# Kernel tuning notes

Hardware: AMD Instinct MI355X
Metric: run time of the kernel (lower is better)

The kernel has to match this reference:

```python
import jax, jax.numpy as jnp
import numpy as np

N_NODES = 100000
N_GRAPHS = 64


def gcn_layer(x, src, dst, W, b, n):
    # GCNConv: h = x @ W; out_i = sum_j norm_ij * h_j (+ self loop), + bias
    h = x @ W
    deg = jax.ops.segment_sum(jnp.ones(src.shape[0], x.dtype), dst, num_segments=n)
    dinv = jnp.where(deg > 0, jax.lax.rsqrt(deg), 0.0)
    norm = dinv[src] * dinv[dst]                      # [E+N]
    agg = jax.ops.segment_sum(h[src] * norm[:, None], dst, num_segments=n)
    return agg + b


def setup_inputs() -> dict:
    key = jax.random.key(0)
    ks = jax.random.split(key, 12)
    nfeat, nhid, nclass = 128, 64, 10
    E = 1600000
    x = jax.random.normal(ks[0], (N_NODES, nfeat), dtype=jnp.float32)
    edge_index = jax.random.randint(ks[1], (2, E), 0, N_NODES, dtype=jnp.int64)
    batch = jnp.sort(jax.random.randint(ks[2], (N_NODES,), 0, N_GRAPHS, dtype=jnp.int64))
    def w(k, fi, fo):
        return jax.random.normal(k, (fi, fo), dtype=jnp.float32) / np.sqrt(fi)
    return {
        "x": x, "edge_index": edge_index, "batch": batch,
        "W1": w(ks[3], nfeat, nhid), "b1": jnp.zeros((nhid,), jnp.float32),
        "W2": w(ks[4], nhid, nhid), "b2": jnp.zeros((nhid,), jnp.float32),
        "W3": w(ks[5], nhid, nhid), "b3": jnp.zeros((nhid,), jnp.float32),
        "Wl": w(ks[6], nhid, nclass), "bl": jnp.zeros((nclass,), jnp.float32),
    }


def reference(x, edge_index, batch, W1, b1, W2, b2, W3, b3, Wl, bl):
    n = x.shape[0]
    loop = jnp.arange(n, dtype=edge_index.dtype)
    src = jnp.concatenate([edge_index[0], loop])   # self-loops appended
    dst = jnp.concatenate([edge_index[1], loop])
    h = x  # eval mode: dropout is identity; use_bn=False
    for W, b in ((W1, b1), (W2, b2), (W3, b3)):
        h = jax.nn.relu(gcn_layer(h, src, dst, W, b, n))
    # global mean pool per graph
    sums = jax.ops.segment_sum(h, batch, num_segments=N_GRAPHS)
    cnts = jax.ops.segment_sum(jnp.ones((n,), h.dtype), batch, num_segments=N_GRAPHS)
    pooled = sums / jnp.maximum(cnts, 1.0)[:, None]   # [G, nhid]
    logits = pooled @ Wl + bl
    return jax.nn.softmax(logits, axis=1)
```

## Files before the change

kernel.cpp:

```cpp
#include <hip/hip_runtime.h>
#include <math.h>


typedef __attribute__((ext_vector_type(8))) short bf16x8;
typedef __attribute__((ext_vector_type(4))) float f32x4;
typedef __attribute__((ext_vector_type(2))) float f32x2;

__device__ __forceinline__ unsigned short f2bf(float f) {
    unsigned int u = __float_as_uint(f);
    u += 0x7fffu + ((u >> 16) & 1u);
    return (unsigned short)(u >> 16);
}
__device__ __forceinline__ float bf2f(unsigned short u) {
    return __uint_as_float((unsigned int)u << 16);
}
__device__ __forceinline__ float bflo(unsigned int u) {
    return __uint_as_float(u << 16);
}
__device__ __forceinline__ float bfhi(unsigned int u) {
    return __uint_as_float(u & 0xffff0000u);
}


__global__ __launch_bounds__(256) void hist_kernel(const int* __restrict__ dst,
                                                   int* __restrict__ counts,
                                                   int E, int P, int C,
                                                   const float* __restrict__ W1,
                                                   const float* __restrict__ W2,
                                                   const float* __restrict__ W3,
                                                   unsigned short* __restrict__ Wt1,
                                                   unsigned short* __restrict__ Wt2,
                                                   unsigned short* __restrict__ Wt3,
                                                   float* __restrict__ sums, int G) {
    int t = threadIdx.x, b = blockIdx.x;
    if (b >= 256) {
        int xb = b - 256;
        if (xb < 3) {
            const float* W = (xb == 0) ? W1 : ((xb == 1) ? W2 : W3);
            unsigned short* Wt = (xb == 0) ? Wt1 : ((xb == 1) ? Wt2 : Wt3);
            int K = (xb == 0) ? 128 : 64;
            int o = t & 63;
            for (int k = t >> 6; k < K; k += 4)
                Wt[o * K + k] = f2bf(W[k * 64 + o]);
        } else {
            for (int i = t; i < G * 65; i += 256) sums[i] = 0.f;
        }
        return;
    }
    __shared__ int hist[256];
    if (t < P) hist[t] = 0;
    __syncthreads();
    int beg = b * C, end = min(E, beg + C);
    for (int e = beg + t; e < end; e += 256)
        atomicAdd(&hist[dst[e] >> 9], 1);
    __syncthreads();
    if (t < P) counts[t * 256 + b] = hist[t];
}

__global__ __launch_bounds__(256) void pscan_kernel(const int* __restrict__ counts,
                                                    int* __restrict__ pbase,
                                                    int P) {
    __shared__ int s[256];
    int t = threadIdx.x;
    int v = 0;
    if (t < P)
        for (int b = 0; b < 256; ++b) v += counts[t * 256 + b];
    s[t] = v;
    __syncthreads();
    for (int off = 1; off < 256; off <<= 1) {
        int u = (t >= off) ? s[t - off] : 0;
        __syncthreads();
        s[t] += u;
        __syncthreads();
    }
    if (t < P) pbase[t] = s[t] - v;
    if (t == 255) pbase[P] = s[255];
}

__global__ __launch_bounds__(256) void offs_kernel(const int* __restrict__ counts,
                                                   const int* __restrict__ pbase,
                                                   int* __restrict__ offs) {
    __shared__ int s[256];
    int t = threadIdx.x, p = blockIdx.x;
    int v = counts[p * 256 + t];
    s[t] = v;
    __syncthreads();
    for (int off = 1; off < 256; off <<= 1) {
        int u = (t >= off) ? s[t - off] : 0;
        __syncthreads();
        s[t] += u;
        __syncthreads();
    }
    offs[p * 256 + t] = pbase[p] + s[t] - v;
}

__global__ __launch_bounds__(256) void bin_kernel(const int* __restrict__ src,
                                                  const int* __restrict__ dst,
                                                  const int* __restrict__ offs,
                                                  unsigned int* __restrict__ binned,
                                                  int E, int P, int C) {
    __shared__ int cur[256];
    int t = threadIdx.x, b = blockIdx.x;
    if (t < P) cur[t] = offs[t * 256 + b];
    __syncthreads();
    int beg = b * C, end = min(E, beg + C);
    for (int e = beg + t; e < end; e += 256) {
        int d = dst[e], s = src[e];
        int pos = atomicAdd(&cur[d >> 9], 1);
        binned[pos] = ((unsigned int)s << 9) | (unsigned int)(d & 511);
    }
}

__global__ __launch_bounds__(512) void lsortA_kernel(const unsigned int* __restrict__ binned,
                                                     const int* __restrict__ pbase,
                                                     float* __restrict__ dinv,
                                                     int* __restrict__ ovfw, int N) {
    __shared__ int ldeg[512];
    __shared__ int s[512];
    int t = threadIdx.x, p = blockIdx.x;
    int lo = p << 9;
    ldeg[t] = 0;
    __syncthreads();
    int eBeg = pbase[p], eEnd = pbase[p + 1];
    for (int j = eBeg + t; j < eEnd; j += 512)
        atomicAdd(&ldeg[binned[j] & 511u], 1);
    __syncthreads();
    int real = ldeg[t];
    int deg1 = real + 1;
    int ovfUsed = (lo + t < N) ? max(deg1 - 24, 0) : 0;
    int gsl = ((ovfUsed + 7) >> 3) << 3;
    s[t] = gsl;
    __syncthreads();
    for (int off = 1; off < 512; off <<= 1) {
        int u = (t >= off) ? s[t - off] : 0;
        __syncthreads();
        s[t] += u;
        __syncthreads();
    }
    if (lo + t < N) {
        dinv[lo + t] = rsqrtf((float)deg1);
        int obase = ((eBeg + 7) & ~7) + (p << 12);
        int base = obase + (s[t] - gsl);
        ovfw[lo + t] = gsl ? (((base >> 3) << 7) | (gsl >> 3)) : 0;
    }
}

__global__ __launch_bounds__(256) void lsortB_kernel(const unsigned int* __restrict__ binned,
                                                     const int* __restrict__ pbase,
                                                     const int* __restrict__ ovfw,
                                                     const float* __restrict__ dinv,
                                                     float2* __restrict__ csrw,
                                                     float2* __restrict__ ovf, int N) {
    __shared__ int cur[512];
    __shared__ float sdi[512];
    __shared__ int sov[512];
    int t = threadIdx.x, p = blockIdx.x;
    int lo = p << 9, span = min(N - lo, 512);
    for (int i = t; i < span; i += 256) {
        cur[i] = 0;
        sdi[i] = dinv[lo + i];
        sov[i] = ovfw[lo + i];
    }
    __syncthreads();
    int eBeg = pbase[p], eEnd = pbase[p + 1];
    for (int j = eBeg + t; j < eEnd; j += 256) {
        unsigned int vv = binned[j];
        int sr = (int)(vv >> 9);
        int dl = (int)(vv & 511u);
        int i = atomicAdd(&cur[dl], 1);
        float2 ent = make_float2(__int_as_float(sr << 7), dinv[sr] * sdi[dl]);
        if (i < 24) csrw[(size_t)(lo + dl) * 24 + i] = ent;
        else        ovf[(size_t)((sov[dl] >> 7) << 3) + i - 24] = ent;
    }
    __syncthreads();
    for (int i = t; i < span; i += 256) {
        int real = cur[i];
        int node = lo + i;
        float d = sdi[i];
        float2 self = make_float2(__int_as_float(node << 7), d * d);
        int deg1 = real + 1;
        int ob = (sov[i] >> 7) << 3;
        if (real < 24) csrw[(size_t)node * 24 + real] = self;
        else           ovf[(size_t)ob + real - 24] = self;
        for (int k = deg1; k < 24; ++k)
            csrw[(size_t)node * 24 + k] = make_float2(0.f, 0.f);
        int gsl = (sov[i] & 127) << 3;
        for (int k = max(deg1 - 24, 0); k < gsl; ++k)
            ovf[(size_t)ob + k] = make_float2(0.f, 0.f);
    }
}

template <int FIN, bool F32IN>
__global__ __launch_bounds__(256) void gemm_mfma_kernel(const void* __restrict__ Xv,
                                                        const unsigned short* __restrict__ Wt,
                                                        unsigned short* __restrict__ H,
                                                        int N) {
    constexpr int KS = FIN / 32;
    constexpr int LDP = FIN + 8;
    __shared__ unsigned short sX[64 * LDP];
    int tid = threadIdx.x;
    int rowBase = blockIdx.x * 64;

    if (F32IN) {
        for (int i = tid * 4; i < 64 * FIN; i += 1024) {
            int r = i / FIN, c = i - r * FIN;
            int gr = min(rowBase + r, N - 1);
            float4 vv = *(const float4*)((const float*)Xv + (size_t)gr * FIN + c);
            unsigned e0 = __float_as_uint(vv.x) + 0x8000u, e1 = __float_as_uint(vv.y) + 0x8000u;
            unsigned e2 = __float_as_uint(vv.z) + 0x8000u, e3 = __float_as_uint(vv.w) + 0x8000u;
            uint2 pk;
            pk.x = __builtin_amdgcn_perm(e1, e0, 0x07060302);
            pk.y = __builtin_amdgcn_perm(e3, e2, 0x07060302);
            *(uint2*)&sX[r * LDP + c] = pk;
        }
    } else {
        for (int i = tid * 8; i < 64 * FIN; i += 2048) {
            int r = i / FIN, c = i - r * FIN;
            int gr = min(rowBase + r, N - 1);
            uint4 vv = *(const uint4*)((const unsigned short*)Xv + (size_t)gr * FIN + c);
            *(uint4*)&sX[r * LDP + c] = vv;
        }
    }
    __syncthreads();

    int wave = tid >> 6;
    int lane = tid & 63;
    int r = lane & 15, g = lane >> 4;
    int node = rowBase + wave * 16 + r;

    bf16x8 afr[4][KS];
#pragma unroll
    for (int m = 0; m < 4; ++m)
#pragma unroll
        for (int s = 0; s < KS; ++s)
            afr[m][s] = *(const bf16x8*)&Wt[(m * 16 + r) * FIN + s * 32 + g * 8];

    f32x4 acc[4];
#pragma unroll
    for (int m = 0; m < 4; ++m) acc[m] = (f32x4){0.f, 0.f, 0.f, 0.f};

#pragma unroll
    for (int s = 0; s < KS; ++s) {
        bf16x8 bfr = *(const bf16x8*)&sX[(wave * 16 + r) * LDP + s * 32 + g * 8];
#pragma unroll
        for (int m = 0; m < 4; ++m)
            acc[m] = __builtin_amdgcn_mfma_f32_16x16x32_bf16(afr[m][s], bfr, acc[m], 0, 0, 0);
    }

    if (node < N) {
#pragma unroll
        for (int m = 0; m < 4; ++m) {
            ushort4 o;
            o.x = f2bf(acc[m][0]); o.y = f2bf(acc[m][1]);
            o.z = f2bf(acc[m][2]); o.w = f2bf(acc[m][3]);
            *(ushort4*)&H[(size_t)node * 64 + m * 16 + g * 4] = o;
        }
    }
}

template <int NQ>
__device__ __forceinline__ void gstep(const float2* __restrict__ csrw,
                                      const char* __restrict__ hb,
                                      int e, int g, int fo, f32x2 acc[4]) {
    float2 c[NQ];
#pragma unroll
    for (int q = 0; q < NQ; ++q) c[q] = csrw[e + 8 * q + g];
    uint4 u[NQ];
#pragma unroll
    for (int q = 0; q < NQ; ++q)
        u[q] = *(const uint4*)(hb + __float_as_int(c[q].x) + fo);
#pragma unroll
    for (int q = 0; q < NQ; ++q) {
        f32x2 w2;
        w2.x = c[q].y; w2.y = c[q].y;
        acc[0] = __builtin_elementwise_fma(w2, (f32x2){bflo(u[q].x), bfhi(u[q].x)}, acc[0]);
        acc[1] = __builtin_elementwise_fma(w2, (f32x2){bflo(u[q].y), bfhi(u[q].y)}, acc[1]);
        acc[2] = __builtin_elementwise_fma(w2, (f32x2){bflo(u[q].z), bfhi(u[q].z)}, acc[2]);
        acc[3] = __builtin_elementwise_fma(w2, (f32x2){bflo(u[q].w), bfhi(u[q].w)}, acc[3]);
    }
}

__global__ __launch_bounds__(256) void gather_kernel(const float2* __restrict__ csrw,
                                                     const float2* __restrict__ ovf,
                                                     const int* __restrict__ ovfw,
                                                     const unsigned short* __restrict__ h,
                                                     const float* __restrict__ b,
                                                     unsigned short* __restrict__ aggb, int N) {
    int node = (blockIdx.x * 256 + threadIdx.x) >> 6;
    int lane = threadIdx.x & 63;
    if (node >= N) return;
    int g = lane >> 3;
    int f = lane & 7;
    int fo = f * 16;

    f32x2 acc[4];
#pragma unroll
    for (int k = 0; k < 4; ++k) acc[k] = (f32x2){0.f, 0.f};

    const char* hb = (const char*)h;
    gstep<3>(csrw, hb, node * 24, g, fo, acc);

    int ow = ovfw[node];
    if (ow) {
        int onb = ow & 127;
        int oe = (ow >> 7) << 3;
        while (onb >= 4) { gstep<4>(ovf, hb, oe, g, fo, acc); oe += 32; onb -= 4; }
        if (onb == 3)      gstep<3>(ovf, hb, oe, g, fo, acc);
        else if (onb == 2) gstep<2>(ovf, hb, oe, g, fo, acc);
        else if (onb == 1) gstep<1>(ovf, hb, oe, g, fo, acc);
    }

    float a[8];
#pragma unroll
    for (int k = 0; k < 4; ++k) { a[2 * k] = acc[k].x; a[2 * k + 1] = acc[k].y; }
#pragma unroll
    for (int k = 0; k < 8; ++k) {
        float v = a[k];
        v += __shfl_xor(v, 8);
        v += __shfl_xor(v, 16);
        v += __shfl_xor(v, 32);
        a[k] = v;
    }
    if (g == 0) {
        float4 bv0 = *(const float4*)&b[f * 8];
        float4 bv1 = *(const float4*)&b[f * 8 + 4];
        float a0 = fmaxf(a[0] + bv0.x, 0.f), a1 = fmaxf(a[1] + bv0.y, 0.f);
        float a2 = fmaxf(a[2] + bv0.z, 0.f), a3 = fmaxf(a[3] + bv0.w, 0.f);
        float a4 = fmaxf(a[4] + bv1.x, 0.f), a5 = fmaxf(a[5] + bv1.y, 0.f);
        float a6 = fmaxf(a[6] + bv1.z, 0.f), a7 = fmaxf(a[7] + bv1.w, 0.f);
        uint4 o;
        o.x = ((unsigned)f2bf(a1) << 16) | f2bf(a0);
        o.y = ((unsigned)f2bf(a3) << 16) | f2bf(a2);
        o.z = ((unsigned)f2bf(a5) << 16) | f2bf(a4);
        o.w = ((unsigned)f2bf(a7) << 16) | f2bf(a6);
        *(uint4*)&aggb[((size_t)node << 6) + f * 8] = o;
    }
}

__global__ __launch_bounds__(256) void pool_kernel(const unsigned short* __restrict__ hb,
                                                   const int* __restrict__ batch,
                                                   float* __restrict__ sums,
                                                   float* __restrict__ cnts, int N) {
    int lane = threadIdx.x & 63;
    int wid = (blockIdx.x * 256 + threadIdx.x) >> 6;
    int base = wid * 32;
    if (base >= N) return;
    int nn = min(N - base, 32);
    int bl = batch[base + min(lane & 31, nn - 1)];

    float v[32];
#pragma unroll
    for (int j = 0; j < 32; ++j) {
        int node = base + min(j, nn - 1);
        v[j] = bf2f(hb[(size_t)node * 64 + lane]);
    }

    int curg = __shfl(bl, 0);
    float acc = 0.f, cnt = 0.f;
#pragma unroll
    for (int j = 0; j < 32; ++j) {
        if (j < nn) {
            int g = __shfl(bl, j);
            if (g != curg) {
                atomicAdd(&sums[curg * 64 + lane], acc);
                if (lane == 0) atomicAdd(&cnts[curg], cnt);
                acc = 0.f; cnt = 0.f; curg = g;
            }
            acc += v[j]; cnt += 1.f;
        }
    }
    atomicAdd(&sums[curg * 64 + lane], acc);
    if (lane == 0) atomicAdd(&cnts[curg], cnt);
}

__global__ void final_kernel(const float* __restrict__ sums, const float* __restrict__ cnts,
                             const float* __restrict__ Wl, const float* __restrict__ bl,
                             float* __restrict__ out, int G) {
    int g = blockIdx.x * blockDim.x + threadIdx.x;
    if (g >= G) return;
    float inv = 1.0f / fmaxf(cnts[g], 1.0f);
    float logits[10];
#pragma unroll
    for (int k = 0; k < 10; ++k) logits[k] = bl[k];
    for (int c = 0; c < 64; ++c) {
        float p = sums[g * 64 + c] * inv;
#pragma unroll
        for (int k = 0; k < 10; ++k) logits[k] = fmaf(p, Wl[c * 10 + k], logits[k]);
    }
    float m = logits[0];
#pragma unroll
    for (int k = 1; k < 10; ++k) m = fmaxf(m, logits[k]);
    float se = 0.f;
#pragma unroll
    for (int k = 0; k < 10; ++k) { logits[k] = expf(logits[k] - m); se += logits[k]; }
    float is = 1.0f / se;
#pragma unroll
    for (int k = 0; k < 10; ++k) out[g * 10 + k] = logits[k] * is;
}

extern "C" void kernel_launch(void* const* d_in, const int* in_sizes, int n_in,
                              void* d_out, int out_size, void* d_ws, size_t ws_size,
                              hipStream_t stream) {
    const float* x    = (const float*)d_in[0];
    const int* edges  = (const int*)d_in[1];
    const int* batch  = (const int*)d_in[2];
    const float* W1   = (const float*)d_in[3];
    const float* b1   = (const float*)d_in[4];
    const float* W2   = (const float*)d_in[5];
    const float* b2   = (const float*)d_in[6];
    const float* W3   = (const float*)d_in[7];
    const float* b3   = (const float*)d_in[8];
    const float* Wl   = (const float*)d_in[9];
    const float* bl   = (const float*)d_in[10];

    const int N = in_sizes[0] / 128;
    const int E = in_sizes[1] / 2;
    const int G = out_size / 10;
    const int* src = edges;
    const int* dst = edges + E;

    float* ws     = (float*)d_ws;
    unsigned short* h = (unsigned short*)ws;
    unsigned short* aggb = (unsigned short*)(ws + (size_t)N * 32);
    unsigned int* binned = (unsigned int*)ws;
    size_t o = (size_t)N * 64;
    float2* csrw  = (float2*)(ws + o);  o += (size_t)48 * N;
    float2* ovf   = (float2*)(ws + o);  o += (size_t)2 * (E + 4096 * 256 + 8);
    float* dinv   = ws + o;            o += N;
    int*   ovfw   = (int*)(ws + o);    o += N;
    int*   counts = (int*)(ws + o);    o += 256 * 256;
    int*   offs   = (int*)(ws + o);    o += 256 * 256;
    int*   pbase  = (int*)(ws + o);    o += 257;
    float* sums   = ws + o;            o += (size_t)G * 64;
    float* cnts   = ws + o;            o += G;
    unsigned short* Wt1 = (unsigned short*)(ws + o);
    unsigned short* Wt2 = Wt1 + 64 * 128;
    unsigned short* Wt3 = Wt2 + 64 * 64;

    const int gemmGrid = (N + 63) / 64;
    const int gatherGrid = (N + 3) / 4;
    const int poolGrid = ((N + 31) / 32 + 3) / 4;
    const int P = (N + 511) >> 9;
    const int C = (E + 255) / 256;

    hist_kernel<<<260, 256, 0, stream>>>(dst, counts, E, P, C,
                                         W1, W2, W3, Wt1, Wt2, Wt3, sums, G);
    pscan_kernel<<<1, 256, 0, stream>>>(counts, pbase, P);
    offs_kernel<<<P, 256, 0, stream>>>(counts, pbase, offs);
    bin_kernel<<<256, 256, 0, stream>>>(src, dst, offs, binned, E, P, C);
    lsortA_kernel<<<P, 512, 0, stream>>>(binned, pbase, dinv, ovfw, N);
    lsortB_kernel<<<P, 256, 0, stream>>>(binned, pbase, ovfw, dinv, csrw, ovf, N);

    gemm_mfma_kernel<128, true><<<gemmGrid, 256, 0, stream>>>(x, Wt1, h, N);
    gather_kernel<<<gatherGrid, 256, 0, stream>>>(csrw, ovf, ovfw, h, b1, aggb, N);

    gemm_mfma_kernel<64, false><<<gemmGrid, 256, 0, stream>>>(aggb, Wt2, h, N);
    gather_kernel<<<gatherGrid, 256, 0, stream>>>(csrw, ovf, ovfw, h, b2, aggb, N);

    gemm_mfma_kernel<64, false><<<gemmGrid, 256, 0, stream>>>(aggb, Wt3, h, N);
    gather_kernel<<<gatherGrid, 256, 0, stream>>>(csrw, ovf, ovfw, h, b3, aggb, N);

    pool_kernel<<<poolGrid, 256, 0, stream>>>(aggb, batch, sums, cnts, N);
    final_kernel<<<1, 64, 0, stream>>>(sums, cnts, Wl, bl, (float*)d_out, G);
}
```

Baseline: 346.9 us.

## Fuse edge binning with first-layer GEMM and drop offsets kernel

Removes the separate offsets-scan kernel: each binning block now computes its per-partition start offsets by summing the counts row serially up to its block index. The binning work and the first-layer x@W1 MFMA GEMM are merged into one launch, with blocks split by index so both run concurrently. The binned buffer moves to the aggb region so it does not overlap h, which the GEMM now writes at the same time. This saves two launches and lets the independent GEMM overlap binning, at the cost of a serial prefix sum of up to 255 loads per thread and more shared memory per block, which may reduce occupancy for the binning blocks.

```diff
diff --git a/kernel.cpp b/kernel.cpp
--- a/kernel.cpp
+++ b/kernel.cpp
@@ -77,37 +77,86 @@
     if (t == 255) pbase[P] = s[255];
 }
 
-__global__ __launch_bounds__(256) void offs_kernel(const int* __restrict__ counts,
-                                                   const int* __restrict__ pbase,
-                                                   int* __restrict__ offs) {
-    __shared__ int s[256];
-    int t = threadIdx.x, p = blockIdx.x;
-    int v = counts[p * 256 + t];
-    s[t] = v;
-    __syncthreads();
-    for (int off = 1; off < 256; off <<= 1) {
-        int u = (t >= off) ? s[t - off] : 0;
+__global__ __launch_bounds__(256) void bin_gemm_kernel(const int* __restrict__ src,
+                                                       const int* __restrict__ dst,
+                                                       const int* __restrict__ counts,
+                                                       const int* __restrict__ pbase,
+                                                       unsigned int* __restrict__ binned,
+                                                       int E, int P, int C,
+                                                       const float* __restrict__ X,
+                                                       const unsigned short* __restrict__ Wt,
+                                                       unsigned short* __restrict__ H, int N) {
+    __shared__ int cur[256];
+    __shared__ unsigned short sX[64 * 136];
+    int t = threadIdx.x, b = blockIdx.x;
+
+    if (b < 256) {
+        if (t < P) {
+            int off = pbase[t];
+            const int* row = counts + t * 256;
+            for (int b2 = 0; b2 < b; ++b2) off += row[b2];
+            cur[t] = off;
+        }
         __syncthreads();
-        s[t] += u;
-        __syncthreads();
-    }
-    offs[p * 256 + t] = pbase[p] + s[t] - v;
-}
-
-__global__ __launch_bounds__(256) void bin_kernel(const int* __restrict__ src,
-                                                  const int* __restrict__ dst,
-                                                  const int* __restrict__ offs,
-                                                  unsigned int* __restrict__ binned,
-                                                  int E, int P, int C) {
-    __shared__ int cur[256];
-    int t = threadIdx.x, b = blockIdx.x;
-    if (t < P) cur[t] = offs[t * 256 + b];
-    __syncthreads();
-    int beg = b * C, end = min(E, beg + C);
-    for (int e = beg + t; e < end; e += 256) {
-        int d = dst[e], s = src[e];
-        int pos = atomicAdd(&cur[d >> 9], 1);
-        binned[pos] = ((unsigned int)s << 9) | (unsigned int)(d & 511);
+        int beg = b * C, end = min(E, beg + C);
+        for (int e = beg + t; e < end; e += 256) {
+            int d = dst[e], s = src[e];
+            int pos = atomicAdd(&cur[d >> 9], 1);
+            binned[pos] = ((unsigned int)s << 9) | (unsigned int)(d & 511);
+        }
+        return;
+    }
+
+    constexpr int FIN = 128;
+    constexpr int KS = FIN / 32;
+    constexpr int LDP = FIN + 8;
+    int rowBase = (b - 256) * 64;
+
+    for (int i = t * 4; i < 64 * FIN; i += 1024) {
+        int r = i / FIN, c = i - r * FIN;
+        int gr = min(rowBase + r, N - 1);
+        float4 vv = *(const float4*)(X + (size_t)gr * FIN + c);
+        unsigned e0 = __float_as_uint(vv.x) + 0x8000u, e1 = __float_as_uint(vv.y) + 0x8000u;
+        unsigned e2 = __float_as_uint(vv.z) + 0x8000u, e3 = __float_as_uint(vv.w) + 0x8000u;
+        uint2 pk;
+        pk.x = __builtin_amdgcn_perm(e1, e0, 0x07060302);
+        pk.y = __builtin_amdgcn_perm(e3, e2, 0x07060302);
+        *(uint2*)&sX[r * LDP + c] = pk;
+    }
+    __syncthreads();
+
+    int wave = t >> 6;
+    int lane = t & 63;
+    int r = lane & 15, g = lane >> 4;
+    int node = rowBase + wave * 16 + r;
+
+    bf16x8 afr[4][KS];
+#pragma unroll
+    for (int m = 0; m < 4; ++m)
+#pragma unroll
+        for (int s = 0; s < KS; ++s)
+            afr[m][s] = *(const bf16x8*)&Wt[(m * 16 + r) * FIN + s * 32 + g * 8];
+
+    f32x4 acc[4];
+#pragma unroll
+    for (int m = 0; m < 4; ++m) acc[m] = (f32x4){0.f, 0.f, 0.f, 0.f};
+
+#pragma unroll
+    for (int s = 0; s < KS; ++s) {
+        bf16x8 bfr = *(const bf16x8*)&sX[(wave * 16 + r) * LDP + s * 32 + g * 8];
+#pragma unroll
+        for (int m = 0; m < 4; ++m)
+            acc[m] = __builtin_amdgcn_mfma_f32_16x16x32_bf16(afr[m][s], bfr, acc[m], 0, 0, 0);
+    }
+
+    if (node < N) {
+#pragma unroll
+        for (int m = 0; m < 4; ++m) {
+            ushort4 o;
+            o.x = f2bf(acc[m][0]); o.y = f2bf(acc[m][1]);
+            o.z = f2bf(acc[m][2]); o.w = f2bf(acc[m][3]);
+            *(ushort4*)&H[(size_t)node * 64 + m * 16 + g * 4] = o;
+        }
     }
 }
 
@@ -190,8 +239,8 @@
     }
 }
 
-template <int FIN, bool F32IN>
-__global__ __launch_bounds__(256) void gemm_mfma_kernel(const void* __restrict__ Xv,
+template <int FIN>
+__global__ __launch_bounds__(256) void gemm_mfma_kernel(const unsigned short* __restrict__ Xv,
                                                         const unsigned short* __restrict__ Wt,
                                                         unsigned short* __restrict__ H,
                                                         int N) {
@@ -201,25 +250,11 @@
     int tid = threadIdx.x;
     int rowBase = blockIdx.x * 64;
 
-    if (F32IN) {
-        for (int i = tid * 4; i < 64 * FIN; i += 1024) {
-            int r = i / FIN, c = i - r * FIN;
-            int gr = min(rowBase + r, N - 1);
-            float4 vv = *(const float4*)((const float*)Xv + (size_t)gr * FIN + c);
-            unsigned e0 = __float_as_uint(vv.x) + 0x8000u, e1 = __float_as_uint(vv.y) + 0x8000u;
-            unsigned e2 = __float_as_uint(vv.z) + 0x8000u, e3 = __float_as_uint(vv.w) + 0x8000u;
-            uint2 pk;
-            pk.x = __builtin_amdgcn_perm(e1, e0, 0x07060302);
-            pk.y = __builtin_amdgcn_perm(e3, e2, 0x07060302);
-            *(uint2*)&sX[r * LDP + c] = pk;
-        }
-    } else {
-        for (int i = tid * 8; i < 64 * FIN; i += 2048) {
-            int r = i / FIN, c = i - r * FIN;
-            int gr = min(rowBase + r, N - 1);
-            uint4 vv = *(const uint4*)((const unsigned short*)Xv + (size_t)gr * FIN + c);
-            *(uint4*)&sX[r * LDP + c] = vv;
-        }
+    for (int i = tid * 8; i < 64 * FIN; i += 2048) {
+        int r = i / FIN, c = i - r * FIN;
+        int gr = min(rowBase + r, N - 1);
+        uint4 vv = *(const uint4*)(Xv + (size_t)gr * FIN + c);
+        *(uint4*)&sX[r * LDP + c] = vv;
     }
     __syncthreads();
 
@@ -422,14 +457,13 @@
     float* ws     = (float*)d_ws;
     unsigned short* h = (unsigned short*)ws;
     unsigned short* aggb = (unsigned short*)(ws + (size_t)N * 32);
-    unsigned int* binned = (unsigned int*)ws;
+    unsigned int* binned = (unsigned int*)(ws + (size_t)N * 32);
     size_t o = (size_t)N * 64;
     float2* csrw  = (float2*)(ws + o);  o += (size_t)48 * N;
     float2* ovf   = (float2*)(ws + o);  o += (size_t)2 * (E + 4096 * 256 + 8);
     float* dinv   = ws + o;            o += N;
     int*   ovfw   = (int*)(ws + o);    o += N;
     int*   counts = (int*)(ws + o);    o += 256 * 256;
-    int*   offs   = (int*)(ws + o);    o += 256 * 256;
     int*   pbase  = (int*)(ws + o);    o += 257;
     float* sums   = ws + o;            o += (size_t)G * 64;
     float* cnts   = ws + o;            o += G;
@@ -446,18 +480,18 @@
     hist_kernel<<<260, 256, 0, stream>>>(dst, counts, E, P, C,
                                          W1, W2, W3, Wt1, Wt2, Wt3, sums, G);
     pscan_kernel<<<1, 256, 0, stream>>>(counts, pbase, P);
-    offs_kernel<<<P, 256, 0, stream>>>(counts, pbase, offs);
-    bin_kernel<<<256, 256, 0, stream>>>(src, dst, offs, binned, E, P, C);
+    bin_gemm_kernel<<<256 + gemmGrid, 256, 0, stream>>>(src, dst, counts, pbase,
+                                                        binned, E, P, C,
+                                                        x, Wt1, h, N);
     lsortA_kernel<<<P, 512, 0, stream>>>(binned, pbase, dinv, ovfw, N);
     lsortB_kernel<<<P, 256, 0, stream>>>(binned, pbase, ovfw, dinv, csrw, ovf, N);
 
-    gemm_mfma_kernel<128, true><<<gemmGrid, 256, 0, stream>>>(x, Wt1, h, N);
     gather_kernel<<<gatherGrid, 256, 0, stream>>>(csrw, ovf, ovfw, h, b1, aggb, N);
 
-    gemm_mfma_kernel<64, false><<<gemmGrid, 256, 0, stream>>>(aggb, Wt2, h, N);
+    gemm_mfma_kernel<64><<<gemmGrid, 256, 0, stream>>>(aggb, Wt2, h, N);
     gather_kernel<<<gatherGrid, 256, 0, stream>>>(csrw, ovf, ovfw, h, b2, aggb, N);
 
-    gemm_mfma_kernel<64, false><<<gemmGrid, 256, 0, stream>>>(aggb, Wt3, h, N);
+    gemm_mfma_kernel<64><<<gemmGrid, 256, 0, stream>>>(aggb, Wt3, h, N);
     gather_kernel<<<gatherGrid, 256, 0, stream>>>(csrw, ovf, ovfw, h, b3, aggb, N);
 
     pool_kernel<<<poolGrid, 256, 0, stream>>>(aggb, batch, sums, cnts, N);
```

After: 358.2 us. 1.03x slower.
